# Performance work log

Measured on AMD Instinct MI355X. Metric: run time of the kernel, lower is better.

The kernel has to match this reference:

```python
import jax, jax.numpy as jnp
import numpy as np

B, N, S = 8, 4096, 1024
D1, D2 = 128, 256
IN_C = D1 + D2
MLP = [256, 256]
BN_EPS = 1e-5


def setup_inputs() -> dict:
    key = jax.random.key(0)
    ks = jax.random.split(key, 32)
    inp = {
        'xyz1': jax.random.uniform(ks[0], (B, 3, N), dtype=jnp.float32),
        'xyz2': jax.random.uniform(ks[1], (B, 3, S), dtype=jnp.float32),
        'points1': jax.random.normal(ks[2], (B, D1, N), dtype=jnp.float32),
        'points2': jax.random.normal(ks[3], (B, D2, S), dtype=jnp.float32),
        'colors1': jax.random.normal(ks[4], (B, D1, N), dtype=jnp.float32),
        'colors2': jax.random.normal(ks[5], (B, D2, S), dtype=jnp.float32),
    }
    # conv1x1 + BN params for the two MLP stacks (points / colors)
    k = 6
    last = IN_C
    for li, out_c in enumerate(MLP, start=1):
        for tag in ('p', 'c'):
            scale = 1.0 / np.sqrt(last)
            inp[f'W{tag}{li}'] = jax.random.uniform(ks[k], (out_c, last), jnp.float32, -scale, scale); k += 1
            inp[f'b{tag}{li}'] = jax.random.uniform(ks[k], (out_c,), jnp.float32, -scale, scale); k += 1
            inp[f'g{tag}{li}'] = jnp.ones((out_c,), jnp.float32)
            inp[f'be{tag}{li}'] = jnp.zeros((out_c,), jnp.float32)
        last = out_c
    return inp


def _square_distance(src, dst):
    # src [B,N,3], dst [B,S,3] -> [B,N,S]
    d = -2.0 * jnp.einsum('bnc,bsc->bns', src, dst)
    d = d + jnp.sum(src * src, -1)[:, :, None]
    d = d + jnp.sum(dst * dst, -1)[:, None, :]
    return d


def _three_interp(xyz1, xyz2, feat2):
    # xyz1 [B,N,3], xyz2 [B,S,3], feat2 [B,S,D] -> [B,N,D]
    dists = _square_distance(xyz1, xyz2)              # [B,N,S]
    neg_d3, idx = jax.lax.top_k(-dists, 3)            # smallest 3 distances
    d3 = -neg_d3                                      # [B,N,3] ascending
    recip = 1.0 / (d3 + 1e-8)
    weight = recip / jnp.sum(recip, axis=2, keepdims=True)
    gathered = jax.vmap(lambda f, i: f[i])(feat2, idx)  # [B,N,3,D]
    return jnp.sum(gathered * weight[..., None], axis=2)


def _conv_bn_relu(x, W, b, g, be):
    # x [B,N,Cin]; conv1x1 == per-point linear; BN in training mode (batch stats)
    y = jnp.einsum('bnc,oc->bno', x, W) + b
    m = jnp.mean(y, axis=(0, 1))
    v = jnp.var(y, axis=(0, 1))
    yn = (y - m) * jax.lax.rsqrt(v + BN_EPS)
    return jax.nn.relu(yn * g + be)


def reference(xyz1, xyz2, points1, points2, colors1, colors2,
              Wp1, bp1, gp1, bep1, Wc1, bc1, gc1, bec1,
              Wp2, bp2, gp2, bep2, Wc2, bc2, gc2, bec2):
    x1 = jnp.transpose(xyz1, (0, 2, 1))   # [B,N,3]
    x2 = jnp.transpose(xyz2, (0, 2, 1))   # [B,S,3]
    p2 = jnp.transpose(points2, (0, 2, 1))  # [B,S,D2]
    c2 = jnp.transpose(colors2, (0, 2, 1))

    interp_p = _three_interp(x1, x2, p2)  # [B,N,D2]
    interp_c = _three_interp(x1, x2, c2)

    p1 = jnp.transpose(points1, (0, 2, 1))  # [B,N,D1]
    c1 = jnp.transpose(colors1, (0, 2, 1))
    new_p = jnp.concatenate([p1, interp_p], axis=-1)  # [B,N,IN_C]
    new_c = jnp.concatenate([c1, interp_c], axis=-1)

    new_p = _conv_bn_relu(new_p, Wp1, bp1, gp1, bep1)
    new_p = _conv_bn_relu(new_p, Wp2, bp2, gp2, bep2)
    new_c = _conv_bn_relu(new_c, Wc1, bc1, gc1, bec1)
    new_c = _conv_bn_relu(new_c, Wc2, bc2, gc2, bec2)

    return (jnp.transpose(new_p, (0, 2, 1)), jnp.transpose(new_c, (0, 2, 1)))
```

## Files before the change

kernel.cpp:

```cpp
#include <hip/hip_runtime.h>
#include <cstdint>
#include <cstddef>


#define B_   8
#define N_   4096
#define S_   1024
#define D1_  128
#define D2_  256
#define INC_ 384
#define OC_  256
#define M_   (B_ * N_)

typedef __attribute__((ext_vector_type(8))) short sh8;
typedef __attribute__((ext_vector_type(4))) float f32x4;
typedef __attribute__((ext_vector_type(4))) unsigned short ush4;
typedef __attribute__((ext_vector_type(8))) unsigned short ush8;

__device__ __forceinline__ unsigned short bf16rne(float f) {
    union { float f; unsigned u; } v; v.f = f;
    return (unsigned short)((v.u + 0x7FFFu + ((v.u >> 16) & 1u)) >> 16);
}
__device__ __forceinline__ float bf2f(unsigned short h) {
    union { unsigned u; float f; } v; v.u = ((unsigned)h) << 16;
    return v.f;
}
__device__ __forceinline__ void gload16(const void* gsrc, void* lds) {
    __builtin_amdgcn_global_load_lds(
        (const __attribute__((address_space(1))) void*)gsrc,
        (__attribute__((address_space(3))) void*)lds, 16, 0, 0);
}

#define INS(pd, pi, d0, d1, d2, i0, i1, i2) { \
    bool l0 = (pd < d0) || (pd == d0 && pi < i0); \
    bool l1 = (pd < d1) || (pd == d1 && pi < i1); \
    bool l2 = (pd < d2) || (pd == d2 && pi < i2); \
    d2 = l1 ? d1 : (l2 ? pd : d2);  i2 = l1 ? i1 : (l2 ? pi : i2); \
    d1 = l0 ? d0 : (l1 ? pd : d1);  i1 = l0 ? i0 : (l1 ? pi : i1); \
    d0 = l0 ? pd : d0;              i0 = l0 ? pi : i0; \
}

__global__ __launch_bounds__(256) void front_kernel(
    const float* __restrict__ xyz1, const float* __restrict__ xyz2,
    const float* __restrict__ points1, const float* __restrict__ colors1,
    const float* __restrict__ points2, const float* __restrict__ colors2,
    const float* __restrict__ Wp1, const float* __restrict__ Wc1,
    const float* __restrict__ Wp2, const float* __restrict__ Wc2,
    int* __restrict__ idxo, float* __restrict__ wo,
    unsigned short* __restrict__ p2b, unsigned short* __restrict__ c2b,
    unsigned short* __restrict__ Wb1, unsigned short* __restrict__ Wb2,
    unsigned short* __restrict__ Xp)
{
    __shared__ __align__(16) char fsm[17664];
    const int bid = blockIdx.x;
    const int tid = threadIdx.x;

    if (bid < 512) {
        float4* sc = (float4*)fsm;
        const int b = bid >> 6, qb = bid & 63;
        const float* x2 = xyz2 + (size_t)b * 3 * S_;
        for (int s = tid; s < S_; s += 256) {
            float xs = x2[s], ys = x2[S_ + s], zs = x2[2 * S_ + s];
            sc[s] = make_float4(xs, ys, zs, xs * xs + ys * ys + zs * zs);
        }
        __syncthreads();
        const int qA = qb * 64 + (tid >> 3);
        const int qB = qA + 32;
        const int sub = tid & 7;
        const float* x1 = xyz1 + (size_t)b * 3 * N_;
        const float xa = x1[qA], ya = x1[N_ + qA], za = x1[2 * N_ + qA];
        const float xb = x1[qB], yb = x1[N_ + qB], zb = x1[2 * N_ + qB];
        const float na = xa * xa + ya * ya + za * za;
        const float nb = xb * xb + yb * yb + zb * zb;
        float ad0 = 3.4e38f, ad1 = 3.4e38f, ad2 = 3.4e38f;
        float bd0 = 3.4e38f, bd1 = 3.4e38f, bd2 = 3.4e38f;
        int ai0 = 0, ai1 = 0, ai2 = 0, bi0 = 0, bi1 = 0, bi2 = 0;
#pragma unroll 4
        for (int j = 0; j < 128; ++j) {
            int s = j * 8 + sub;
            float4 v = sc[s];
            float da = (na - 2.0f * (xa * v.x + ya * v.y + za * v.z)) + v.w;
            float db = (nb - 2.0f * (xb * v.x + yb * v.y + zb * v.z)) + v.w;
            bool a0 = da < ad0, a1 = da < ad1, a2 = da < ad2;
            ad2 = a1 ? ad1 : (a2 ? da : ad2); ai2 = a1 ? ai1 : (a2 ? s : ai2);
            ad1 = a0 ? ad0 : (a1 ? da : ad1); ai1 = a0 ? ai0 : (a1 ? s : ai1);
            ad0 = a0 ? da : ad0;              ai0 = a0 ? s : ai0;
            bool b0 = db < bd0, b1 = db < bd1, b2 = db < bd2;
            bd2 = b1 ? bd1 : (b2 ? db : bd2); bi2 = b1 ? bi1 : (b2 ? s : bi2);
            bd1 = b0 ? bd0 : (b1 ? db : bd1); bi1 = b0 ? bi0 : (b1 ? s : bi1);
            bd0 = b0 ? db : bd0;              bi0 = b0 ? s : bi0;
        }
#pragma unroll
        for (int off = 1; off < 8; off <<= 1) {
            float p0 = __shfl_xor(ad0, off), p1 = __shfl_xor(ad1, off), p2 = __shfl_xor(ad2, off);
            int   j0 = __shfl_xor(ai0, off), j1 = __shfl_xor(ai1, off), j2 = __shfl_xor(ai2, off);
            INS(p0, j0, ad0, ad1, ad2, ai0, ai1, ai2)
            INS(p1, j1, ad0, ad1, ad2, ai0, ai1, ai2)
            INS(p2, j2, ad0, ad1, ad2, ai0, ai1, ai2)
            float q0 = __shfl_xor(bd0, off), q1 = __shfl_xor(bd1, off), q2 = __shfl_xor(bd2, off);
            int   k0 = __shfl_xor(bi0, off), k1 = __shfl_xor(bi1, off), k2 = __shfl_xor(bi2, off);
            INS(q0, k0, bd0, bd1, bd2, bi0, bi1, bi2)
            INS(q1, k1, bd0, bd1, bd2, bi0, bi1, bi2)
            INS(q2, k2, bd0, bd1, bd2, bi0, bi1, bi2)
        }
        if (sub == 0) {
            {
                float r0 = 1.f / (ad0 + 1e-8f);
                float r1 = 1.f / (ad1 + 1e-8f);
                float r2 = 1.f / (ad2 + 1e-8f);
                float rs = r0 + r1 + r2;
                int base = (b * N_ + qA) * 3;
                idxo[base] = ai0; idxo[base + 1] = ai1; idxo[base + 2] = ai2;
                wo[base] = r0 / rs; wo[base + 1] = r1 / rs; wo[base + 2] = r2 / rs;
            }
            {
                float r0 = 1.f / (bd0 + 1e-8f);
                float r1 = 1.f / (bd1 + 1e-8f);
                float r2 = 1.f / (bd2 + 1e-8f);
                float rs = r0 + r1 + r2;
                int base = (b * N_ + qB) * 3;
                idxo[base] = bi0; idxo[base + 1] = bi1; idxo[base + 2] = bi2;
                wo[base] = r0 / rs; wo[base + 1] = r1 / rs; wo[base + 2] = r2 / rs;
            }
        }
    } else if (bid < 1024) {
        float (*tile)[33] = (float(*)[33])fsm;
        const int u = bid - 512;
        const int which = u >> 8;
        const int v = u & 255;
        const int z = v >> 5, cx = v & 31;
        const int tx = tid & 31, ty = tid >> 5;
        const float* s = (which ? colors2 : points2) + (size_t)z * D2_ * S_;
        unsigned short* d = (which ? c2b : p2b) + (size_t)z * S_ * D2_;
        for (int ry = 0; ry < 8; ++ry) {
            if (ry) __syncthreads();
#pragma unroll
            for (int i = 0; i < 4; ++i)
                tile[ty + i * 8][tx] = s[(size_t)(ry * 32 + ty + i * 8) * S_ + cx * 32 + tx];
            __syncthreads();
#pragma unroll
            for (int i = 0; i < 4; ++i)
                d[(size_t)(cx * 32 + ty + i * 8) * D2_ + ry * 32 + tx] =
                    bf16rne(tile[tx][ty + i * 8]);
        }
    } else if (bid < 1344) {
        int e = ((bid - 1024) * 256 + tid) * 4;
        const float* src; unsigned short* dst; int off;
        if (e < 98304)       { src = Wp1; dst = Wb1;          off = e; }
        else if (e < 196608) { src = Wc1; dst = Wb1 + 98304;  off = e - 98304; }
        else if (e < 262144) { src = Wp2; dst = Wb2;          off = e - 196608; }
        else                 { src = Wc2; dst = Wb2 + 65536;  off = e - 262144; }
        float4 v = *(const float4*)(src + off);
        ush4 o; o[0] = bf16rne(v.x); o[1] = bf16rne(v.y); o[2] = bf16rne(v.z); o[3] = bf16rne(v.w);
        *(ush4*)(dst + off) = o;
    } else {
        float (*tileA)[69] = (float(*)[69])fsm;
        const int u = bid - 1344;
        const int t = u >> 9, rem = u & 511;
        const int b = rem >> 6, n0 = (rem & 63) * 64;
        const float* x1 = t ? colors1 : points1;
        size_t mbase = (size_t)t * M_ + (size_t)b * N_ + n0;
#pragma unroll
        for (int ph = 0; ph < 2; ++ph) {
            if (ph) __syncthreads();
#pragma unroll
            for (int it = 0; it < 4; ++it) {
                int fl4 = it * 256 + tid;
                int dl = fl4 >> 4, nl = (fl4 & 15) * 4;
                float4 v = *(const float4*)(x1 + ((size_t)b * D1_ + ph * 64 + dl) * N_ + n0 + nl);
                tileA[nl][dl] = v.x; tileA[nl + 1][dl] = v.y;
                tileA[nl + 2][dl] = v.z; tileA[nl + 3][dl] = v.w;
            }
            __syncthreads();
#pragma unroll
            for (int it = 0; it < 2; ++it) {
                int e8 = it * 256 + tid;
                int r = e8 >> 3, dc = (e8 & 7) * 8;
                ush8 o;
#pragma unroll
                for (int j = 0; j < 8; ++j) o[j] = bf16rne(tileA[r][dc + j]);
                *(ush8*)(Xp + (mbase + r) * D1_ + ph * 64 + dc) = o;
            }
        }
    }
}

__global__ __launch_bounds__(512, 2) void gemm1f_kernel(
    const unsigned short* __restrict__ Xp,
    const unsigned short* __restrict__ p2b,
    const unsigned short* __restrict__ c2b,
    const int* __restrict__ idxw, const float* __restrict__ wgtw,
    const unsigned short* __restrict__ Wb1,
    unsigned short* __restrict__ Y1,
    float* __restrict__ psum, float* __restrict__ psq)
{
    const int wg  = blockIdx.x;
    const int xcd = wg & 7;
    const int t   = xcd & 1;
    const int mt  = (xcd >> 1) * 32 + (wg >> 3);
    const int m0  = mt * 256;
    const int bb  = m0 >> 12;
    const unsigned short* Aw  = Wb1 + (size_t)t * (OC_ * INC_);
    const unsigned short* Xb  = Xp + (size_t)t * M_ * D1_;
    const unsigned short* f2b = t ? c2b : p2b;

    __shared__ __align__(16) char smem[65536];

    const int tid  = threadIdx.x;
    const int lane = tid & 63;
    const int wid  = tid >> 6;
    const int wc   = wid & 3;
    const int wm   = wid >> 2;
    const int srow = tid >> 3;
    const int k8   = (tid & 7) * 8;
    const int sk   = ((tid & 7) ^ (srow & 7)) * 8;
    const int kgrp = (lane >> 4) * 16;

    int gi[4][3]; float gw[4][3];
#pragma unroll
    for (int p = 0; p < 4; ++p) {
        int base = (m0 + p * 64 + srow) * 3;
#pragma unroll
        for (int j = 0; j < 3; ++j) { gi[p][j] = idxw[base + j]; gw[p][j] = wgtw[base + j]; }
    }

    f32x4 acc[4][8];
#pragma unroll
    for (int i = 0; i < 4; ++i)
#pragma unroll
        for (int j = 0; j < 8; ++j) acc[i][j] = f32x4{0.f, 0.f, 0.f, 0.f};

    auto stageA = [&](int kc) {
#pragma unroll
        for (int p = 0; p < 4; ++p)
            gload16(Aw + (size_t)(p * 64 + srow) * INC_ + kc + sk,
                    smem + p * 8192 + wid * 1024);
    };
    auto stageBX = [&](int kc) {
#pragma unroll
        for (int p = 0; p < 4; ++p)
            gload16(Xb + (size_t)(m0 + p * 64 + srow) * D1_ + kc + sk,
                    smem + 32768 + p * 8192 + wid * 1024);
    };
    auto stageBG = [&](int kc) {
        const int d0k = kc - D1_ + k8;
#pragma unroll
        for (int p = 0; p < 4; ++p) {
            int row = p * 64 + srow;
            ush8 a0 = *(const ush8*)(f2b + ((size_t)bb * S_ + gi[p][0]) * D2_ + d0k);
            ush8 a1 = *(const ush8*)(f2b + ((size_t)bb * S_ + gi[p][1]) * D2_ + d0k);
            ush8 a2 = *(const ush8*)(f2b + ((size_t)bb * S_ + gi[p][2]) * D2_ + d0k);
            ush8 ov;
#pragma unroll
            for (int j = 0; j < 8; ++j)
                ov[j] = bf16rne(gw[p][0] * bf2f(a0[j]) + gw[p][1] * bf2f(a1[j])
                              + gw[p][2] * bf2f(a2[j]));
            *(ush8*)(smem + 32768 + row * 128 + ((k8 * 2) ^ ((row & 7) << 4))) = ov;
        }
    };
    auto compute = [&]() {
#pragma unroll
        for (int kk = 0; kk < 2; ++kk) {
            sh8 a[4], b[8];
#pragma unroll
            for (int f = 0; f < 4; ++f) {
                int ra = wc * 64 + (lane & 15) + f * 16;
                a[f] = *(const sh8*)(smem + ra * 128
                        + ((kk * 64 + kgrp) ^ ((ra & 7) << 4)));
            }
#pragma unroll
            for (int f = 0; f < 8; ++f) {
                int rb = wm * 128 + (lane & 15) + f * 16;
                b[f] = *(const sh8*)(smem + 32768 + rb * 128
                        + ((kk * 64 + kgrp) ^ ((rb & 7) << 4)));
            }
#pragma unroll
            for (int fc = 0; fc < 4; ++fc)
#pragma unroll
                for (int fm = 0; fm < 8; ++fm)
                    acc[fc][fm] = __builtin_amdgcn_mfma_f32_16x16x32_bf16(
                        a[fc], b[fm], acc[fc][fm], 0, 0, 0);
        }
    };

    for (int step = 0; step < 6; ++step) {
        int kc = step * 64;
        if (step) __syncthreads();
        stageA(kc);
        if (kc < D1_) stageBX(kc);
        else          stageBG(kc);
        __syncthreads();
        compute();
    }
    __syncthreads();

    const int mrow = m0 + wm * 128 + (lane & 15);
    const int chq  = (lane >> 4) * 4;
#pragma unroll
    for (int fm = 0; fm < 8; ++fm)
#pragma unroll
        for (int fc = 0; fc < 4; ++fc) {
            ush4 v;
#pragma unroll
            for (int r = 0; r < 4; ++r) v[r] = bf16rne(acc[fc][fm][r]);
            *(ush4*)(Y1 + ((size_t)t * M_ + mrow + fm * 16) * OC_
                      + wc * 64 + fc * 16 + chq) = v;
        }

    float* sArr = (float*)smem;
    const int contrib = wm * 16 + (lane & 15);
#pragma unroll
    for (int ph = 0; ph < 2; ++ph) {
#pragma unroll
        for (int fc = 0; fc < 4; ++fc) {
            f32x4 s4;
#pragma unroll
            for (int r = 0; r < 4; ++r) {
                float s = 0.f;
#pragma unroll
                for (int fm = 0; fm < 8; ++fm) { float v = acc[fc][fm][r]; s += ph ? v * v : v; }
                s4[r] = s;
            }
            *(f32x4*)&sArr[contrib * 264 + wc * 64 + fc * 16 + chq] = s4;
        }
        __syncthreads();
        if (tid < 256) {
            float s = 0.f;
#pragma unroll
            for (int k = 0; k < 32; ++k) s += sArr[((k + tid) & 31) * 264 + tid];
            (ph ? psq : psum)[((size_t)t * 128 + mt) * 256 + tid] = s;
        }
        __syncthreads();
    }
}

__global__ __launch_bounds__(256) void reduce_kernel(
    const float* __restrict__ psum, const float* __restrict__ psq,
    const float* __restrict__ gp, const float* __restrict__ bep,
    const float* __restrict__ gc, const float* __restrict__ bec,
    float* __restrict__ ss, int layerOff)
{
    const int t = blockIdx.x, cs = blockIdx.y;
    const int tid = threadIdx.x;
    const int cl = tid & 63, grp = tid >> 6;
    const int c = cs * 64 + cl;
    float s = 0.f, q = 0.f;
    for (int k = grp; k < 128; k += 4) {
        s += psum[((size_t)t * 128 + k) * 256 + c];
        q += psq [((size_t)t * 128 + k) * 256 + c];
    }
    __shared__ float ls[4][64], lq[4][64];
    ls[grp][cl] = s; lq[grp][cl] = q;
    __syncthreads();
    if (tid < 64) {
        s = ls[0][cl] + ls[1][cl] + ls[2][cl] + ls[3][cl];
        q = lq[0][cl] + lq[1][cl] + lq[2][cl] + lq[3][cl];
        float mean = s * (1.f / (float)M_);
        float var  = q * (1.f / (float)M_) - mean * mean;
        float inv  = rsqrtf(var + 1e-5f);
        float g = (t ? gc : gp)[c], be = (t ? bec : bep)[c];
        float sc = g * inv;
        ss[layerOff + t * 256 + c]       = sc;
        ss[layerOff + 512 + t * 256 + c] = be - mean * sc;
    }
}

__global__ __launch_bounds__(512, 2) void gemm2f_kernel(
    const unsigned short* __restrict__ Y1,
    const unsigned short* __restrict__ Wb2,
    const float* __restrict__ ss,
    unsigned short* __restrict__ y2b,
    float* __restrict__ psum, float* __restrict__ psq)
{
    const int wg  = blockIdx.x;
    const int xcd = wg & 7;
    const int t   = xcd & 1;
    const int mt  = (xcd >> 1) * 32 + (wg >> 3);
    const int m0  = mt * 256;
    const unsigned short* Aw = Wb2 + (size_t)t * (OC_ * OC_);
    const unsigned short* By = Y1 + (size_t)t * M_ * OC_;

    __shared__ __align__(16) char smem[65536];
    __shared__ float Slds[256], Hlds[256];

    const int tid  = threadIdx.x;
    const int lane = tid & 63;
    const int wid  = tid >> 6;
    const int wc   = wid & 3;
    const int wm   = wid >> 2;
    const int srow = tid >> 3;
    const int k8   = (tid & 7) * 8;
    const int sk   = ((tid & 7) ^ (srow & 7)) * 8;
    const int kgrp = (lane >> 4) * 16;

    if (tid < 256) { Slds[tid] = ss[t * 256 + tid]; Hlds[tid] = ss[512 + t * 256 + tid]; }
    __syncthreads();

    f32x4 acc[4][8];
#pragma unroll
    for (int i = 0; i < 4; ++i)
#pragma unroll
        for (int j = 0; j < 8; ++j) acc[i][j] = f32x4{0.f, 0.f, 0.f, 0.f};

    auto stageA = [&](int kc) {
#pragma unroll
        for (int p = 0; p < 4; ++p)
            gload16(Aw + (size_t)(p * 64 + srow) * OC_ + kc + sk,
                    smem + p * 8192 + wid * 1024);
    };
    auto stageBY = [&](int kc) {
#pragma unroll
        for (int p = 0; p < 4; ++p) {
            int row = p * 64 + srow;
            ush8 yv = *(const ush8*)(By + (size_t)(m0 + row) * OC_ + kc + k8);
            ush8 ov;
#pragma unroll
            for (int j = 0; j < 8; ++j) {
                float y = bf2f(yv[j]);
                ov[j] = bf16rne(fmaxf(0.f, fmaf(y, Slds[kc + k8 + j], Hlds[kc + k8 + j])));
            }
            *(ush8*)(smem + 32768 + row * 128 + ((k8 * 2) ^ ((row & 7) << 4))) = ov;
        }
    };
    auto compute = [&]() {
#pragma unroll
        for (int kk = 0; kk < 2; ++kk) {
            sh8 a[4], b[8];
#pragma unroll
            for (int f = 0; f < 4; ++f) {
                int ra = wc * 64 + (lane & 15) + f * 16;
                a[f] = *(const sh8*)(smem + ra * 128
                        + ((kk * 64 + kgrp) ^ ((ra & 7) << 4)));
            }
#pragma unroll
            for (int f = 0; f < 8; ++f) {
                int rb = wm * 128 + (lane & 15) + f * 16;
                b[f] = *(const sh8*)(smem + 32768 + rb * 128
                        + ((kk * 64 + kgrp) ^ ((rb & 7) << 4)));
            }
#pragma unroll
            for (int fc = 0; fc < 4; ++fc)
#pragma unroll
                for (int fm = 0; fm < 8; ++fm)
                    acc[fc][fm] = __builtin_amdgcn_mfma_f32_16x16x32_bf16(
                        a[fc], b[fm], acc[fc][fm], 0, 0, 0);
        }
    };

    for (int step = 0; step < 4; ++step) {
        int kc = step * 64;
        if (step) __syncthreads();
        stageA(kc);
        stageBY(kc);
        __syncthreads();
        compute();
    }
    __syncthreads();

    const int mrow = m0 + wm * 128 + (lane & 15);
    const int chq  = (lane >> 4) * 4;
#pragma unroll
    for (int fm = 0; fm < 8; ++fm)
#pragma unroll
        for (int fc = 0; fc < 4; ++fc) {
            ush4 v;
#pragma unroll
            for (int r = 0; r < 4; ++r) v[r] = bf16rne(acc[fc][fm][r]);
            *(ush4*)(y2b + ((size_t)t * M_ + mrow + fm * 16) * OC_
                      + wc * 64 + fc * 16 + chq) = v;
        }

    float* sArr = (float*)smem;
    const int contrib = wm * 16 + (lane & 15);
#pragma unroll
    for (int ph = 0; ph < 2; ++ph) {
#pragma unroll
        for (int fc = 0; fc < 4; ++fc) {
            f32x4 s4;
#pragma unroll
            for (int r = 0; r < 4; ++r) {
                float s = 0.f;
#pragma unroll
                for (int fm = 0; fm < 8; ++fm) { float v = acc[fc][fm][r]; s += ph ? v * v : v; }
                s4[r] = s;
            }
            *(f32x4*)&sArr[contrib * 264 + wc * 64 + fc * 16 + chq] = s4;
        }
        __syncthreads();
        if (tid < 256) {
            float s = 0.f;
#pragma unroll
            for (int k = 0; k < 32; ++k) s += sArr[((k + tid) & 31) * 264 + tid];
            (ph ? psq : psum)[((size_t)t * 128 + mt) * 256 + tid] = s;
        }
        __syncthreads();
    }
}

__global__ __launch_bounds__(256) void bnT_kernel(
    const unsigned short* __restrict__ y2b, const float* __restrict__ ss,
    float* __restrict__ out)
{
    const int z = blockIdx.z;
    const int t = z >> 3, b = z & 7;
    const int o0 = blockIdx.y * 64;
    const int n0 = blockIdx.x * 64;
    const int tid = threadIdx.x;
    __shared__ unsigned short tile[64][72];

    const unsigned short* src = y2b + ((size_t)t * M_ + (size_t)b * N_ + n0) * OC_ + o0;
#pragma unroll
    for (int it = 0; it < 2; ++it) {
        int u = it * 256 + tid;
        int m_l = u >> 3, o8 = (u & 7) * 8;
        *(ush8*)&tile[m_l][o8] = *(const ush8*)(src + (size_t)m_l * OC_ + o8);
    }
    __syncthreads();
#pragma unroll
    for (int it = 0; it < 4; ++it) {
        int v = it * 256 + tid;
        int o_l = v >> 4, n4 = (v & 15) * 4;
        int o = o0 + o_l;
        float sc = ss[1024 + t * 256 + o];
        float sh = ss[1536 + t * 256 + o];
        float4 w;
        w.x = fmaxf(0.f, fmaf(bf2f(tile[n4][o_l]),     sc, sh));
        w.y = fmaxf(0.f, fmaf(bf2f(tile[n4 + 1][o_l]), sc, sh));
        w.z = fmaxf(0.f, fmaf(bf2f(tile[n4 + 2][o_l]), sc, sh));
        w.w = fmaxf(0.f, fmaf(bf2f(tile[n4 + 3][o_l]), sc, sh));
        *(float4*)(out + (((size_t)t * B_ + b) * OC_ + o) * N_ + n0 + n4) = w;
    }
}

extern "C" void kernel_launch(void* const* d_in, const int* in_sizes, int n_in,
                              void* d_out, int out_size, void* d_ws, size_t ws_size,
                              hipStream_t stream)
{
    const float* xyz1    = (const float*)d_in[0];
    const float* xyz2    = (const float*)d_in[1];
    const float* points1 = (const float*)d_in[2];
    const float* points2 = (const float*)d_in[3];
    const float* colors1 = (const float*)d_in[4];
    const float* colors2 = (const float*)d_in[5];
    const float* Wp1  = (const float*)d_in[6];
    const float* gp1  = (const float*)d_in[8];
    const float* bep1 = (const float*)d_in[9];
    const float* Wc1  = (const float*)d_in[10];
    const float* gc1  = (const float*)d_in[12];
    const float* bec1 = (const float*)d_in[13];
    const float* Wp2  = (const float*)d_in[14];
    const float* gp2  = (const float*)d_in[16];
    const float* bep2 = (const float*)d_in[17];
    const float* Wc2  = (const float*)d_in[18];
    const float* gc2  = (const float*)d_in[20];
    const float* bec2 = (const float*)d_in[21];

    char* ws = (char*)d_ws;
    unsigned short* y2b  = (unsigned short*)(ws + 0);
    unsigned short* Xp   = (unsigned short*)(ws + 0);
    unsigned short* p2b  = (unsigned short*)(ws + 16777216);
    unsigned short* c2b  = (unsigned short*)(ws + 20971520);
    int*   idxw = (int*)  (ws + 25165824);
    float* wgtw = (float*)(ws + 25559040);
    unsigned short* Y1   = (unsigned short*)(ws + 33554432);
    unsigned short* Wb1  = (unsigned short*)(ws + 67108864);
    unsigned short* Wb2  = (unsigned short*)(ws + 67895296);
    float* psum = (float*)(ws + 68419584);
    float* psq  = (float*)(ws + 68681728);
    float* ssb  = (float*)(ws + 68943872);
    float* out  = (float*)d_out;

    front_kernel<<<2368, 256, 0, stream>>>(xyz1, xyz2, points1, colors1,
                                           points2, colors2, Wp1, Wc1, Wp2, Wc2,
                                           idxw, wgtw, p2b, c2b, Wb1, Wb2, Xp);
    gemm1f_kernel<<<256, 512, 0, stream>>>(Xp, p2b, c2b, idxw, wgtw,
                                           Wb1, Y1, psum, psq);
    reduce_kernel<<<dim3(2, 4), 256, 0, stream>>>(psum, psq, gp1, bep1, gc1, bec1, ssb, 0);
    gemm2f_kernel<<<256, 512, 0, stream>>>(Y1, Wb2, ssb, y2b, psum, psq);
    reduce_kernel<<<dim3(2, 4), 256, 0, stream>>>(psum, psq, gp2, bep2, gc2, bec2, ssb, 1024);
    bnT_kernel<<<dim3(64, 4, 16), 256, 0, stream>>>(y2b, ssb, out);
}
```

Baseline: 120.6 us.

## Double-buffer LDS tiles in both GEMM kernels to overlap loads with MFMA

Both fused GEMM kernels move from a single 64 KB LDS stage to a double-buffered 128 KB layout. The next K-chunk (weights plus gathered/interpolated or BN-applied activations) is staged while MFMAs run on the current chunk, and the syncs per step drop from two to one. The goal is to hide global-load and gather latency behind matrix math. The cost is occupancy: launch bounds fall from 2 to 1 workgroups per CU, and 128 KB of LDS leaves room for only one 512-thread block per CU.

```diff
diff --git a/kernel.cpp b/kernel.cpp
--- a/kernel.cpp
+++ b/kernel.cpp
@@ -185,7 +185,7 @@
     }
 }
 
-__global__ __launch_bounds__(512, 2) void gemm1f_kernel(
+__global__ __launch_bounds__(512, 1) void gemm1f_kernel(
     const unsigned short* __restrict__ Xp,
     const unsigned short* __restrict__ p2b,
     const unsigned short* __restrict__ c2b,
@@ -204,7 +204,7 @@
     const unsigned short* Xb  = Xp + (size_t)t * M_ * D1_;
     const unsigned short* f2b = t ? c2b : p2b;
 
-    __shared__ __align__(16) char smem[65536];
+    __shared__ __align__(16) char smem[131072];
 
     const int tid  = threadIdx.x;
     const int lane = tid & 63;
@@ -230,19 +230,19 @@
 #pragma unroll
         for (int j = 0; j < 8; ++j) acc[i][j] = f32x4{0.f, 0.f, 0.f, 0.f};
 
-    auto stageA = [&](int kc) {
+    auto stageA = [&](int buf, int kc) {
 #pragma unroll
         for (int p = 0; p < 4; ++p)
             gload16(Aw + (size_t)(p * 64 + srow) * INC_ + kc + sk,
-                    smem + p * 8192 + wid * 1024);
-    };
-    auto stageBX = [&](int kc) {
+                    smem + buf * 32768 + p * 8192 + wid * 1024);
+    };
+    auto stageBX = [&](int buf, int kc) {
 #pragma unroll
         for (int p = 0; p < 4; ++p)
             gload16(Xb + (size_t)(m0 + p * 64 + srow) * D1_ + kc + sk,
-                    smem + 32768 + p * 8192 + wid * 1024);
-    };
-    auto stageBG = [&](int kc) {
+                    smem + 65536 + buf * 32768 + p * 8192 + wid * 1024);
+    };
+    auto stageBG = [&](int buf, int kc) {
         const int d0k = kc - D1_ + k8;
 #pragma unroll
         for (int p = 0; p < 4; ++p) {
@@ -255,23 +255,24 @@
             for (int j = 0; j < 8; ++j)
                 ov[j] = bf16rne(gw[p][0] * bf2f(a0[j]) + gw[p][1] * bf2f(a1[j])
                               + gw[p][2] * bf2f(a2[j]));
-            *(ush8*)(smem + 32768 + row * 128 + ((k8 * 2) ^ ((row & 7) << 4))) = ov;
-        }
-    };
-    auto compute = [&]() {
+            *(ush8*)(smem + 65536 + buf * 32768 + row * 128
+                     + ((k8 * 2) ^ ((row & 7) << 4))) = ov;
+        }
+    };
+    auto compute = [&](int buf) {
 #pragma unroll
         for (int kk = 0; kk < 2; ++kk) {
             sh8 a[4], b[8];
 #pragma unroll
             for (int f = 0; f < 4; ++f) {
                 int ra = wc * 64 + (lane & 15) + f * 16;
-                a[f] = *(const sh8*)(smem + ra * 128
+                a[f] = *(const sh8*)(smem + buf * 32768 + ra * 128
                         + ((kk * 64 + kgrp) ^ ((ra & 7) << 4)));
             }
 #pragma unroll
             for (int f = 0; f < 8; ++f) {
                 int rb = wm * 128 + (lane & 15) + f * 16;
-                b[f] = *(const sh8*)(smem + 32768 + rb * 128
+                b[f] = *(const sh8*)(smem + 65536 + buf * 32768 + rb * 128
                         + ((kk * 64 + kgrp) ^ ((rb & 7) << 4)));
             }
 #pragma unroll
@@ -283,16 +284,20 @@
         }
     };
 
+    stageA(0, 0); stageBX(0, 0);
+    __syncthreads();
+    int cur = 0;
     for (int step = 0; step < 6; ++step) {
-        int kc = step * 64;
-        if (step) __syncthreads();
-        stageA(kc);
-        if (kc < D1_) stageBX(kc);
-        else          stageBG(kc);
-        __syncthreads();
-        compute();
-    }
-    __syncthreads();
+        int kcn = (step + 1) * 64;
+        if (step < 5) {
+            stageA(cur ^ 1, kcn);
+            if (kcn < D1_) stageBX(cur ^ 1, kcn);
+            else           stageBG(cur ^ 1, kcn);
+        }
+        compute(cur);
+        __syncthreads();
+        cur ^= 1;
+    }
 
     const int mrow = m0 + wm * 128 + (lane & 15);
     const int chq  = (lane >> 4) * 4;
@@ -365,7 +370,7 @@
     }
 }
 
-__global__ __launch_bounds__(512, 2) void gemm2f_kernel(
+__global__ __launch_bounds__(512, 1) void gemm2f_kernel(
     const unsigned short* __restrict__ Y1,
     const unsigned short* __restrict__ Wb2,
     const float* __restrict__ ss,
@@ -380,7 +385,7 @@
     const unsigned short* Aw = Wb2 + (size_t)t * (OC_ * OC_);
     const unsigned short* By = Y1 + (size_t)t * M_ * OC_;
 
-    __shared__ __align__(16) char smem[65536];
+    __shared__ __align__(16) char smem[131072];
     __shared__ float Slds[256], Hlds[256];
 
     const int tid  = threadIdx.x;
@@ -402,13 +407,13 @@
 #pragma unroll
         for (int j = 0; j < 8; ++j) acc[i][j] = f32x4{0.f, 0.f, 0.f, 0.f};
 
-    auto stageA = [&](int kc) {
+    auto stageA = [&](int buf, int kc) {
 #pragma unroll
         for (int p = 0; p < 4; ++p)
             gload16(Aw + (size_t)(p * 64 + srow) * OC_ + kc + sk,
-                    smem + p * 8192 + wid * 1024);
-    };
-    auto stageBY = [&](int kc) {
+                    smem + buf * 32768 + p * 8192 + wid * 1024);
+    };
+    auto stageBY = [&](int buf, int kc) {
 #pragma unroll
         for (int p = 0; p < 4; ++p) {
             int row = p * 64 + srow;
@@ -419,23 +424,24 @@
                 float y = bf2f(yv[j]);
                 ov[j] = bf16rne(fmaxf(0.f, fmaf(y, Slds[kc + k8 + j], Hlds[kc + k8 + j])));
             }
-            *(ush8*)(smem + 32768 + row * 128 + ((k8 * 2) ^ ((row & 7) << 4))) = ov;
-        }
-    };
-    auto compute = [&]() {
+            *(ush8*)(smem + 65536 + buf * 32768 + row * 128
+                     + ((k8 * 2) ^ ((row & 7) << 4))) = ov;
+        }
+    };
+    auto compute = [&](int buf) {
 #pragma unroll
         for (int kk = 0; kk < 2; ++kk) {
             sh8 a[4], b[8];
 #pragma unroll
             for (int f = 0; f < 4; ++f) {
                 int ra = wc * 64 + (lane & 15) + f * 16;
-                a[f] = *(const sh8*)(smem + ra * 128
+                a[f] = *(const sh8*)(smem + buf * 32768 + ra * 128
                         + ((kk * 64 + kgrp) ^ ((ra & 7) << 4)));
             }
 #pragma unroll
             for (int f = 0; f < 8; ++f) {
                 int rb = wm * 128 + (lane & 15) + f * 16;
-                b[f] = *(const sh8*)(smem + 32768 + rb * 128
+                b[f] = *(const sh8*)(smem + 65536 + buf * 32768 + rb * 128
                         + ((kk * 64 + kgrp) ^ ((rb & 7) << 4)));
             }
 #pragma unroll
@@ -447,15 +453,16 @@
         }
     };
 
+    stageA(0, 0); stageBY(0, 0);
+    __syncthreads();
+    int cur = 0;
     for (int step = 0; step < 4; ++step) {
-        int kc = step * 64;
-        if (step) __syncthreads();
-        stageA(kc);
-        stageBY(kc);
-        __syncthreads();
-        compute();
-    }
-    __syncthreads();
+        int kcn = (step + 1) * 64;
+        if (step < 3) { stageA(cur ^ 1, kcn); stageBY(cur ^ 1, kcn); }
+        compute(cur);
+        __syncthreads();
+        cur ^= 1;
+    }
 
     const int mrow = m0 + wm * 128 + (lane & 15);
     const int chq  = (lane >> 4) * 4;
```

Result: faster. 117.8 us (-2.3%).
